# Kernel tuning notes

Hardware: AMD Instinct MI355X
Metric: run time of the kernel (lower is better)

Reference implementation:

```python
import jax, jax.numpy as jnp
import numpy as np

B = 8192            # graphs per batch
NODES = 54          # Catan board vertices (hard-coded in module)
E_PER = 144         # directed edges per graph (~72 undirected)
IN_DIM, HID_DIM, OUT_DIM, GLOB_DIM = 16, 64, 4, 16


def setup_inputs() -> dict:
    key = jax.random.key(0)
    ks = jax.random.split(key, 20)
    N = B * NODES
    E = B * E_PER

    x = jax.random.normal(ks[0], (N, IN_DIM), dtype=jnp.float32)
    # random intra-graph edges, offset per graph
    src_local = jax.random.randint(ks[1], (B, E_PER), 0, NODES)
    dst_local = jax.random.randint(ks[2], (B, E_PER), 0, NODES)
    offset = (jnp.arange(B, dtype=jnp.int32) * NODES)[:, None]
    edge_index = jnp.stack([
        (src_local + offset).reshape(-1).astype(jnp.int32),
        (dst_local + offset).reshape(-1).astype(jnp.int32),
    ], axis=0)
    edge_attr = jax.random.uniform(ks[3], (E,), dtype=jnp.float32)
    global_feats = jax.random.normal(ks[4], (B, GLOB_DIM), dtype=jnp.float32)

    def lin(k, fan_in, fan_out):
        s = 1.0 / np.sqrt(fan_in)
        k1, k2 = jax.random.split(k)
        W = jax.random.uniform(k1, (fan_in, fan_out), minval=-s, maxval=s, dtype=jnp.float32)
        b = jax.random.uniform(k2, (fan_out,), minval=-s, maxval=s, dtype=jnp.float32)
        return W, b

    # GraphConv layer 1: lin_rel (bias) + lin_root (no bias)
    W1_rel, b1 = lin(ks[5], IN_DIM, HID_DIM)
    W1_root, _ = lin(ks[6], IN_DIM, HID_DIM)
    # GraphConv layer 2
    W2_rel, b2 = lin(ks[7], HID_DIM, OUT_DIM)
    W2_root, _ = lin(ks[8], HID_DIM, OUT_DIM)
    # Global MLP: glob->8->8->glob
    G1_W, G1_b = lin(ks[9], GLOB_DIM, 8)
    G2_W, G2_b = lin(ks[10], 8, 8)
    G3_W, G3_b = lin(ks[11], 8, GLOB_DIM)
    # Out MLP: (54*4+glob)->128->1
    O1_W, O1_b = lin(ks[12], NODES * OUT_DIM + GLOB_DIM, 128)
    O2_W, O2_b = lin(ks[13], 128, 1)

    return dict(x=x, edge_index=edge_index, edge_attr=edge_attr,
                global_feats=global_feats,
                W1_rel=W1_rel, b1=b1, W1_root=W1_root,
                W2_rel=W2_rel, b2=b2, W2_root=W2_root,
                G1_W=G1_W, G1_b=G1_b, G2_W=G2_W, G2_b=G2_b,
                G3_W=G3_W, G3_b=G3_b, O1_W=O1_W, O1_b=O1_b,
                O2_W=O2_W, O2_b=O2_b)


def _graph_conv(x, src, dst, w, W_rel, b_rel, W_root, N):
    # PyG GraphConv (aggr='add'): out_i = W_rel @ sum_j w_ji * x_j + W_root @ x_i + b
    msg = x[src] * w[:, None]                      # [E, d] gather
    agg = jax.ops.segment_sum(msg, dst, num_segments=N)  # [N, d] scatter-add
    return agg @ W_rel + b_rel + x @ W_root


def reference(x, edge_index, edge_attr, global_feats,
              W1_rel, b1, W1_root, W2_rel, b2, W2_root,
              G1_W, G1_b, G2_W, G2_b, G3_W, G3_b,
              O1_W, O1_b, O2_W, O2_b):
    N = x.shape[0]
    src, dst = edge_index[0], edge_index[1]
    h = jax.nn.relu(_graph_conv(x, src, dst, edge_attr, W1_rel, b1, W1_root, N))
    h = jax.nn.relu(_graph_conv(h, src, dst, edge_attr, W2_rel, b2, W2_root, N))
    embeds = h.reshape(N // NODES, NODES * OUT_DIM)          # [B, 216]

    g = jax.nn.relu(global_feats @ G1_W + G1_b)
    g = jax.nn.relu(g @ G2_W + G2_b)
    g = jax.nn.relu(g @ G3_W + G3_b)

    out = jnp.concatenate([embeds, g], axis=-1)              # [B, 232]
    # isTrain=False -> dropout is identity
    out = jax.nn.relu(out @ O1_W + O1_b)
    out = jax.nn.sigmoid(out @ O2_W + O2_b)
    return out
```

## Files before the change

kernel.cpp:

```cpp
#include <hip/hip_runtime.h>
#include <math.h>


#define B_GR 8192
#define NNODE 54
#define EPG 144
#define CATD 232
#define ETOT (B_GR*EPG)
#define WPB 8
#define XS 20
#define PS 12

__global__ __launch_bounds__(512, 4) void conv_kernel(
    const float* __restrict__ x, const int* __restrict__ ei,
    const float* __restrict__ ea, const float* __restrict__ gf,
    const float* __restrict__ W1rel, const float* __restrict__ b1,
    const float* __restrict__ W1root,
    const float* __restrict__ W2rel, const float* __restrict__ b2,
    const float* __restrict__ W2root,
    const float* __restrict__ G1W, const float* __restrict__ G1b,
    const float* __restrict__ G2W, const float* __restrict__ G2b,
    const float* __restrict__ G3W, const float* __restrict__ G3b,
    float* __restrict__ cat)
{
    __shared__ __align__(16) float sW1t[64*36];
    __shared__ __align__(16) float sW2[64*8];
    __shared__ float sb2[4];
    __shared__ __align__(16) float x_s[WPB][NNODE*XS];
    __shared__ __align__(16) float p2_s[WPB][NNODE*PS];
    __shared__ int   ssrc[WPB][EPG];
    __shared__ float sw_ [WPB][EPG];
    __shared__ int   scur[WPB][56];

    const int tid = threadIdx.x;
    const int wg  = tid >> 6;
    const int ln  = tid & 63;
    const int g   = blockIdx.x * WPB + wg;
    const int nbase = g * NNODE;

    for (int i = tid; i < 64*16; i += 512) {
        int d = i & 63, k = i >> 6;
        sW1t[d*36 + k]      = W1rel[k*64 + d];
        sW1t[d*36 + 16 + k] = W1root[k*64 + d];
    }
    if (tid < 64) sW1t[tid*36 + 32] = b1[tid];
    for (int i = tid; i < 64*4; i += 512) {
        int d = i >> 2, j = i & 3;
        sW2[d*8 + j]     = W2rel[i];
        sW2[d*8 + 4 + j] = W2root[i];
    }
    if (tid < 4) sb2[tid] = b2[tid];

    float4 xr[4];
    if (ln < NNODE) {
        const float4* xp = (const float4*)(x + (size_t)(nbase + ln) * 16);
        #pragma unroll
        for (int q = 0; q < 4; q++) {
            xr[q] = xp[q];
            *(float4*)&x_s[wg][ln*XS + q*4] = xr[q];
        }
    }
    int e_src[3], e_dst[3]; float e_w[3];
    #pragma unroll
    for (int r = 0; r < 3; r++) {
        int e = ln + r*64;
        if (e < EPG) {
            e_src[r] = ei[(size_t)g*EPG + e] - nbase;
            e_dst[r] = ei[(size_t)ETOT + (size_t)g*EPG + e] - nbase;
            e_w[r]   = ea[(size_t)g*EPG + e];
        } else e_dst[r] = -1;
    }
    if (ln < NNODE) scur[wg][ln] = 0;
    __builtin_amdgcn_wave_barrier();
    #pragma unroll
    for (int r = 0; r < 3; r++)
        if (e_dst[r] >= 0) atomicAdd(&scur[wg][e_dst[r]], 1);
    __builtin_amdgcn_wave_barrier();
    int c = (ln < NNODE) ? scur[wg][ln] : 0;
    int s = c;
    #pragma unroll
    for (int off = 1; off < 64; off <<= 1) {
        int t = __shfl_up(s, off);
        if (ln >= off) s += t;
    }
    const int deg = c, base = s - c;
    if (ln < NNODE) scur[wg][ln] = base;
    __builtin_amdgcn_wave_barrier();
    #pragma unroll
    for (int r = 0; r < 3; r++)
        if (e_dst[r] >= 0) {
            int pos = atomicAdd(&scur[wg][e_dst[r]], 1);
            ssrc[wg][pos] = e_src[r];
            sw_ [wg][pos] = e_w[r];
        }

    {
        float g1v = 0.f;
        if (ln < 8) {
            float a = G1b[ln];
            #pragma unroll
            for (int k = 0; k < 16; k++) a += gf[(size_t)g*16 + k] * G1W[k*8 + ln];
            g1v = fmaxf(a, 0.f);
        }
        float a2 = (ln < 8) ? G2b[ln] : 0.f;
        #pragma unroll
        for (int k = 0; k < 8; k++) a2 += __shfl(g1v, k) * G2W[k*8 + (ln & 7)];
        float g2v = fmaxf(a2, 0.f);
        float a3 = (ln < 16) ? G3b[ln] : 0.f;
        #pragma unroll
        for (int k = 0; k < 8; k++) a3 += __shfl(g2v, k) * G3W[k*16 + (ln & 15)];
        if (ln < 16) cat[(size_t)g*CATD + 216 + ln] = fmaxf(a3, 0.f);
    }
    __syncthreads();

    float4 a4[4] = {{0,0,0,0},{0,0,0,0},{0,0,0,0},{0,0,0,0}};
    for (int e2 = 0; e2 < deg; e2++) {
        int sv = ssrc[wg][base + e2];
        float w = sw_[wg][base + e2];
        const float4* rp = (const float4*)&x_s[wg][sv*XS];
        #pragma unroll
        for (int q = 0; q < 4; q++) {
            float4 v = rp[q];
            a4[q].x += w*v.x; a4[q].y += w*v.y; a4[q].z += w*v.z; a4[q].w += w*v.w;
        }
    }

    float4 pr0 = {0,0,0,0}, pr1 = {0,0,0,0};
    for (int d = 0; d < 64; d++) {
        const float4* wp = (const float4*)&sW1t[d*36];
        float h = sW1t[d*36 + 32];
        #pragma unroll
        for (int q = 0; q < 4; q++) {
            float4 wv = wp[q];
            h += a4[q].x*wv.x + a4[q].y*wv.y + a4[q].z*wv.z + a4[q].w*wv.w;
        }
        #pragma unroll
        for (int q = 0; q < 4; q++) {
            float4 wv = wp[4+q];
            h += xr[q].x*wv.x + xr[q].y*wv.y + xr[q].z*wv.z + xr[q].w*wv.w;
        }
        h = fmaxf(h, 0.f);
        float4 u0 = *(const float4*)&sW2[d*8];
        float4 u1 = *(const float4*)&sW2[d*8 + 4];
        pr0.x += h*u0.x; pr0.y += h*u0.y; pr0.z += h*u0.z; pr0.w += h*u0.w;
        pr1.x += h*u1.x; pr1.y += h*u1.y; pr1.z += h*u1.z; pr1.w += h*u1.w;
    }
    if (ln < NNODE) *(float4*)&p2_s[wg][ln*PS] = pr0;
    __syncthreads();

    if (ln < NNODE) {
        float4 a2 = {0,0,0,0};
        for (int e2 = 0; e2 < deg; e2++) {
            int sv = ssrc[wg][base + e2];
            float w = sw_[wg][base + e2];
            float4 p = *(const float4*)&p2_s[wg][sv*PS];
            a2.x += w*p.x; a2.y += w*p.y; a2.z += w*p.z; a2.w += w*p.w;
        }
        float4 o;
        o.x = fmaxf(a2.x + pr1.x + sb2[0], 0.f);
        o.y = fmaxf(a2.y + pr1.y + sb2[1], 0.f);
        o.z = fmaxf(a2.z + pr1.z + sb2[2], 0.f);
        o.w = fmaxf(a2.w + pr1.w + sb2[3], 0.f);
        *(float4*)&cat[(size_t)g*CATD + ln*4] = o;
    }
}

__global__ __launch_bounds__(256) void out_kernel(
    const float* __restrict__ cat, const float* __restrict__ O1W,
    const float* __restrict__ O1b, const float* __restrict__ O2W,
    const float* __restrict__ O2b, float* __restrict__ out)
{
    __shared__ __align__(16) float semb[8*CATD];
    __shared__ float sout1[8*132];
    __shared__ float sO1b[128];
    __shared__ float sO2w[128];

    const int tid = threadIdx.x;
    const size_t gbase = (size_t)blockIdx.x * 8;

    for (int i = tid; i < 8*CATD; i += 256) semb[i] = cat[gbase*CATD + i];
    if (tid < 128) { sO1b[tid] = O1b[tid]; sO2w[tid] = O2W[tid]; }
    __syncthreads();

    const int o = tid & 127, gs = tid >> 7;
    float acc[4];
    #pragma unroll
    for (int i = 0; i < 4; i++) acc[i] = sO1b[o];
    const float* eb = &semb[(gs*4)*CATD];
    for (int k = 0; k < CATD; k += 4) {
        float w0 = O1W[(size_t)(k+0)*128 + o];
        float w1 = O1W[(size_t)(k+1)*128 + o];
        float w2 = O1W[(size_t)(k+2)*128 + o];
        float w3 = O1W[(size_t)(k+3)*128 + o];
        #pragma unroll
        for (int i = 0; i < 4; i++) {
            float4 v = *(const float4*)&eb[i*CATD + k];
            acc[i] += v.x*w0 + v.y*w1 + v.z*w2 + v.w*w3;
        }
    }
    #pragma unroll
    for (int i = 0; i < 4; i++) sout1[(gs*4 + i)*132 + o] = fmaxf(acc[i], 0.f);
    __syncthreads();

    if (tid < 8) {
        float a = O2b[0];
        const float* r = &sout1[tid*132];
        for (int oo = 0; oo < 128; oo++) a += r[oo] * sO2w[oo];
        out[gbase + tid] = 1.f / (1.f + expf(-a));
    }
}

extern "C" void kernel_launch(void* const* d_in, const int* in_sizes, int n_in,
                              void* d_out, int out_size, void* d_ws, size_t ws_size,
                              hipStream_t stream) {
    const float* x      = (const float*)d_in[0];
    const int*   ei     = (const int*)d_in[1];
    const float* ea     = (const float*)d_in[2];
    const float* gf     = (const float*)d_in[3];
    const float* W1rel  = (const float*)d_in[4];
    const float* b1     = (const float*)d_in[5];
    const float* W1root = (const float*)d_in[6];
    const float* W2rel  = (const float*)d_in[7];
    const float* b2     = (const float*)d_in[8];
    const float* W2root = (const float*)d_in[9];
    const float* G1W    = (const float*)d_in[10];
    const float* G1b    = (const float*)d_in[11];
    const float* G2W    = (const float*)d_in[12];
    const float* G2b    = (const float*)d_in[13];
    const float* G3W    = (const float*)d_in[14];
    const float* G3b    = (const float*)d_in[15];
    const float* O1W    = (const float*)d_in[16];
    const float* O1b    = (const float*)d_in[17];
    const float* O2W    = (const float*)d_in[18];
    const float* O2b    = (const float*)d_in[19];
    float* out = (float*)d_out;
    float* cat = (float*)d_ws;

    conv_kernel<<<dim3(B_GR/WPB), dim3(512), 0, stream>>>(
        x, ei, ea, gf, W1rel, b1, W1root, W2rel, b2, W2root,
        G1W, G1b, G2W, G2b, G3W, G3b, cat);
    out_kernel<<<dim3(B_GR/8), dim3(256), 0, stream>>>(
        cat, O1W, O1b, O2W, O2b, out);
}
```

Baseline: 195.0 us.

## Prepack conv weights in global memory, drop block syncs, widen output MLP tiles

A tiny prepack kernel writes the layer-1 and layer-2 weights, transposed and interleaved, into a workspace buffer. The conv kernel then reads them with wave-uniform global loads instead of staging them into LDS in every block, which lets the block-wide syncthreads become wave barriers. Edge src and weight are packed into one int2 LDS entry. The output kernel handles 16 graphs per block instead of 8 and spreads the final dot product across lanes with shuffles. This trades an extra launch and cache-dependent scalar/global weight loads for lower LDS footprint and fewer syncs.

```diff
diff --git a/kernel.cpp b/kernel.cpp
--- a/kernel.cpp
+++ b/kernel.cpp
@@ -10,46 +10,50 @@
 #define WPB 8
 #define XS 20
 #define PS 12
+#define WROW 48
+
+__global__ __launch_bounds__(64) void prepack_kernel(
+    const float* __restrict__ W1rel, const float* __restrict__ b1,
+    const float* __restrict__ W1root,
+    const float* __restrict__ W2rel, const float* __restrict__ W2root,
+    float* __restrict__ wpack)
+{
+    const int d = threadIdx.x;
+    float* r = wpack + d * WROW;
+    #pragma unroll
+    for (int k = 0; k < 16; k++) {
+        r[k]      = W1rel[k*64 + d];
+        r[16 + k] = W1root[k*64 + d];
+    }
+    r[32] = b1[d];
+    #pragma unroll
+    for (int j = 0; j < 4; j++) {
+        r[33 + j] = W2rel[d*4 + j];
+        r[37 + j] = W2root[d*4 + j];
+    }
+    #pragma unroll
+    for (int j = 41; j < WROW; j++) r[j] = 0.f;
+}
 
 __global__ __launch_bounds__(512, 4) void conv_kernel(
     const float* __restrict__ x, const int* __restrict__ ei,
     const float* __restrict__ ea, const float* __restrict__ gf,
-    const float* __restrict__ W1rel, const float* __restrict__ b1,
-    const float* __restrict__ W1root,
-    const float* __restrict__ W2rel, const float* __restrict__ b2,
-    const float* __restrict__ W2root,
+    const float* __restrict__ wpack, const float* __restrict__ b2,
     const float* __restrict__ G1W, const float* __restrict__ G1b,
     const float* __restrict__ G2W, const float* __restrict__ G2b,
     const float* __restrict__ G3W, const float* __restrict__ G3b,
     float* __restrict__ cat)
 {
-    __shared__ __align__(16) float sW1t[64*36];
-    __shared__ __align__(16) float sW2[64*8];
-    __shared__ float sb2[4];
     __shared__ __align__(16) float x_s[WPB][NNODE*XS];
     __shared__ __align__(16) float p2_s[WPB][NNODE*PS];
-    __shared__ int   ssrc[WPB][EPG];
-    __shared__ float sw_ [WPB][EPG];
-    __shared__ int   scur[WPB][56];
+    __shared__ __align__(16) int2  sedge[WPB][EPG];
+    __shared__ int scur[WPB][56];
 
     const int tid = threadIdx.x;
     const int wg  = tid >> 6;
     const int ln  = tid & 63;
     const int g   = blockIdx.x * WPB + wg;
     const int nbase = g * NNODE;
-
-    for (int i = tid; i < 64*16; i += 512) {
-        int d = i & 63, k = i >> 6;
-        sW1t[d*36 + k]      = W1rel[k*64 + d];
-        sW1t[d*36 + 16 + k] = W1root[k*64 + d];
-    }
-    if (tid < 64) sW1t[tid*36 + 32] = b1[tid];
-    for (int i = tid; i < 64*4; i += 512) {
-        int d = i >> 2, j = i & 3;
-        sW2[d*8 + j]     = W2rel[i];
-        sW2[d*8 + 4 + j] = W2root[i];
-    }
-    if (tid < 4) sb2[tid] = b2[tid];
 
     float4 xr[4];
     if (ln < NNODE) {
@@ -70,7 +74,7 @@
             e_w[r]   = ea[(size_t)g*EPG + e];
         } else e_dst[r] = -1;
     }
-    if (ln < NNODE) scur[wg][ln] = 0;
+    if (ln < 56) scur[wg][ln] = 0;
     __builtin_amdgcn_wave_barrier();
     #pragma unroll
     for (int r = 0; r < 3; r++)
@@ -90,8 +94,7 @@
     for (int r = 0; r < 3; r++)
         if (e_dst[r] >= 0) {
             int pos = atomicAdd(&scur[wg][e_dst[r]], 1);
-            ssrc[wg][pos] = e_src[r];
-            sw_ [wg][pos] = e_w[r];
+            sedge[wg][pos] = make_int2(e_src[r], __float_as_int(e_w[r]));
         }
 
     {
@@ -111,13 +114,13 @@
         for (int k = 0; k < 8; k++) a3 += __shfl(g2v, k) * G3W[k*16 + (ln & 15)];
         if (ln < 16) cat[(size_t)g*CATD + 216 + ln] = fmaxf(a3, 0.f);
     }
-    __syncthreads();
+    __builtin_amdgcn_wave_barrier();
 
     float4 a4[4] = {{0,0,0,0},{0,0,0,0},{0,0,0,0},{0,0,0,0}};
     for (int e2 = 0; e2 < deg; e2++) {
-        int sv = ssrc[wg][base + e2];
-        float w = sw_[wg][base + e2];
-        const float4* rp = (const float4*)&x_s[wg][sv*XS];
+        int2 se = sedge[wg][base + e2];
+        float w = __int_as_float(se.y);
+        const float4* rp = (const float4*)&x_s[wg][se.x*XS];
         #pragma unroll
         for (int q = 0; q < 4; q++) {
             float4 v = rp[q];
@@ -126,88 +129,95 @@
     }
 
     float4 pr0 = {0,0,0,0}, pr1 = {0,0,0,0};
+    #pragma unroll 2
     for (int d = 0; d < 64; d++) {
-        const float4* wp = (const float4*)&sW1t[d*36];
-        float h = sW1t[d*36 + 32];
-        #pragma unroll
-        for (int q = 0; q < 4; q++) {
-            float4 wv = wp[q];
-            h += a4[q].x*wv.x + a4[q].y*wv.y + a4[q].z*wv.z + a4[q].w*wv.w;
-        }
-        #pragma unroll
-        for (int q = 0; q < 4; q++) {
-            float4 wv = wp[4+q];
-            h += xr[q].x*wv.x + xr[q].y*wv.y + xr[q].z*wv.z + xr[q].w*wv.w;
-        }
+        const float* wr = wpack + d*WROW;
+        float h = wr[32];
+        h += a4[0].x*wr[0]  + a4[0].y*wr[1]  + a4[0].z*wr[2]  + a4[0].w*wr[3];
+        h += a4[1].x*wr[4]  + a4[1].y*wr[5]  + a4[1].z*wr[6]  + a4[1].w*wr[7];
+        h += a4[2].x*wr[8]  + a4[2].y*wr[9]  + a4[2].z*wr[10] + a4[2].w*wr[11];
+        h += a4[3].x*wr[12] + a4[3].y*wr[13] + a4[3].z*wr[14] + a4[3].w*wr[15];
+        h += xr[0].x*wr[16] + xr[0].y*wr[17] + xr[0].z*wr[18] + xr[0].w*wr[19];
+        h += xr[1].x*wr[20] + xr[1].y*wr[21] + xr[1].z*wr[22] + xr[1].w*wr[23];
+        h += xr[2].x*wr[24] + xr[2].y*wr[25] + xr[2].z*wr[26] + xr[2].w*wr[27];
+        h += xr[3].x*wr[28] + xr[3].y*wr[29] + xr[3].z*wr[30] + xr[3].w*wr[31];
         h = fmaxf(h, 0.f);
-        float4 u0 = *(const float4*)&sW2[d*8];
-        float4 u1 = *(const float4*)&sW2[d*8 + 4];
-        pr0.x += h*u0.x; pr0.y += h*u0.y; pr0.z += h*u0.z; pr0.w += h*u0.w;
-        pr1.x += h*u1.x; pr1.y += h*u1.y; pr1.z += h*u1.z; pr1.w += h*u1.w;
+        pr0.x += h*wr[33]; pr0.y += h*wr[34]; pr0.z += h*wr[35]; pr0.w += h*wr[36];
+        pr1.x += h*wr[37]; pr1.y += h*wr[38]; pr1.z += h*wr[39]; pr1.w += h*wr[40];
     }
     if (ln < NNODE) *(float4*)&p2_s[wg][ln*PS] = pr0;
-    __syncthreads();
+    __builtin_amdgcn_wave_barrier();
 
     if (ln < NNODE) {
         float4 a2 = {0,0,0,0};
         for (int e2 = 0; e2 < deg; e2++) {
-            int sv = ssrc[wg][base + e2];
-            float w = sw_[wg][base + e2];
-            float4 p = *(const float4*)&p2_s[wg][sv*PS];
+            int2 se = sedge[wg][base + e2];
+            float w = __int_as_float(se.y);
+            float4 p = *(const float4*)&p2_s[wg][se.x*PS];
             a2.x += w*p.x; a2.y += w*p.y; a2.z += w*p.z; a2.w += w*p.w;
         }
         float4 o;
-        o.x = fmaxf(a2.x + pr1.x + sb2[0], 0.f);
-        o.y = fmaxf(a2.y + pr1.y + sb2[1], 0.f);
-        o.z = fmaxf(a2.z + pr1.z + sb2[2], 0.f);
-        o.w = fmaxf(a2.w + pr1.w + sb2[3], 0.f);
+        o.x = fmaxf(a2.x + pr1.x + b2[0], 0.f);
+        o.y = fmaxf(a2.y + pr1.y + b2[1], 0.f);
+        o.z = fmaxf(a2.z + pr1.z + b2[2], 0.f);
+        o.w = fmaxf(a2.w + pr1.w + b2[3], 0.f);
         *(float4*)&cat[(size_t)g*CATD + ln*4] = o;
     }
 }
+
+#define OG 16
 
 __global__ __launch_bounds__(256) void out_kernel(
     const float* __restrict__ cat, const float* __restrict__ O1W,
     const float* __restrict__ O1b, const float* __restrict__ O2W,
     const float* __restrict__ O2b, float* __restrict__ out)
 {
-    __shared__ __align__(16) float semb[8*CATD];
-    __shared__ float sout1[8*132];
-    __shared__ float sO1b[128];
+    __shared__ __align__(16) float semb[OG*CATD];
+    __shared__ float sout1[OG*132];
     __shared__ float sO2w[128];
 
     const int tid = threadIdx.x;
-    const size_t gbase = (size_t)blockIdx.x * 8;
-
-    for (int i = tid; i < 8*CATD; i += 256) semb[i] = cat[gbase*CATD + i];
-    if (tid < 128) { sO1b[tid] = O1b[tid]; sO2w[tid] = O2W[tid]; }
+    const size_t gbase = (size_t)blockIdx.x * OG;
+
+    for (int i = tid; i < OG*CATD; i += 256) semb[i] = cat[gbase*CATD + i];
+    if (tid < 128) sO2w[tid] = O2W[tid];
     __syncthreads();
 
     const int o = tid & 127, gs = tid >> 7;
-    float acc[4];
-    #pragma unroll
-    for (int i = 0; i < 4; i++) acc[i] = sO1b[o];
-    const float* eb = &semb[(gs*4)*CATD];
-    for (int k = 0; k < CATD; k += 4) {
-        float w0 = O1W[(size_t)(k+0)*128 + o];
-        float w1 = O1W[(size_t)(k+1)*128 + o];
-        float w2 = O1W[(size_t)(k+2)*128 + o];
-        float w3 = O1W[(size_t)(k+3)*128 + o];
-        #pragma unroll
-        for (int i = 0; i < 4; i++) {
-            float4 v = *(const float4*)&eb[i*CATD + k];
-            acc[i] += v.x*w0 + v.y*w1 + v.z*w2 + v.w*w3;
-        }
-    }
-    #pragma unroll
-    for (int i = 0; i < 4; i++) sout1[(gs*4 + i)*132 + o] = fmaxf(acc[i], 0.f);
+    {
+        const float bias = O1b[o];
+        float acc[8];
+        #pragma unroll
+        for (int i = 0; i < 8; i++) acc[i] = bias;
+        const float* eb = &semb[(gs*8)*CATD];
+        for (int k = 0; k < CATD; k += 4) {
+            float w0 = O1W[(size_t)(k+0)*128 + o];
+            float w1 = O1W[(size_t)(k+1)*128 + o];
+            float w2 = O1W[(size_t)(k+2)*128 + o];
+            float w3 = O1W[(size_t)(k+3)*128 + o];
+            #pragma unroll
+            for (int i = 0; i < 8; i++) {
+                float4 v = *(const float4*)&eb[i*CATD + k];
+                acc[i] += v.x*w0 + v.y*w1 + v.z*w2 + v.w*w3;
+            }
+        }
+        #pragma unroll
+        for (int i = 0; i < 8; i++) sout1[(gs*8 + i)*132 + o] = fmaxf(acc[i], 0.f);
+    }
     __syncthreads();
 
-    if (tid < 8) {
-        float a = O2b[0];
-        const float* r = &sout1[tid*132];
-        for (int oo = 0; oo < 128; oo++) a += r[oo] * sO2w[oo];
-        out[gbase + tid] = 1.f / (1.f + expf(-a));
-    }
+    float a = 0.f;
+    const int gg = tid >> 3, t8 = tid & 7;
+    if (tid < 128) {
+        const float* r = &sout1[gg*132];
+        #pragma unroll
+        for (int oo = t8; oo < 128; oo += 8) a += r[oo] * sO2w[oo];
+    }
+    a += __shfl_xor(a, 1);
+    a += __shfl_xor(a, 2);
+    a += __shfl_xor(a, 4);
+    if (tid < 128 && t8 == 0)
+        out[gbase + gg] = 1.f / (1.f + expf(-(a + O2b[0])));
 }
 
 extern "C" void kernel_launch(void* const* d_in, const int* in_sizes, int n_in,
@@ -234,11 +244,14 @@
     const float* O2W    = (const float*)d_in[18];
     const float* O2b    = (const float*)d_in[19];
     float* out = (float*)d_out;
-    float* cat = (float*)d_ws;
-
+    float* cat   = (float*)d_ws;
+    float* wpack = (float*)((char*)d_ws + (size_t)B_GR*CATD*4);
+
+    prepack_kernel<<<dim3(1), dim3(64), 0, stream>>>(
+        W1rel, b1, W1root, W2rel, W2root, wpack);
     conv_kernel<<<dim3(B_GR/WPB), dim3(512), 0, stream>>>(
-        x, ei, ea, gf, W1rel, b1, W1root, W2rel, b2, W2root,
+        x, ei, ea, gf, wpack, b2,
         G1W, G1b, G2W, G2b, G3W, G3b, cat);
-    out_kernel<<<dim3(B_GR/8), dim3(256), 0, stream>>>(
+    out_kernel<<<dim3(B_GR/OG), dim3(256), 0, stream>>>(
         cat, O1W, O1b, O2W, O2b, out);
 }
```

Result: faster. 181.7 us (-6.8%).
